# Performance work log

Hardware: AMD Instinct MI355X
Metric: run time of the kernel (lower is better)

The kernel has to match this reference:

```python
import jax, jax.numpy as jnp
import numpy as np

N, D, C, O = 65536, 256, 1024, 64

def setup_inputs() -> dict:
    key = jax.random.key(0)
    k1, k2, k3, k4 = jax.random.split(key, 4)
    x = jax.random.normal(k1, (N, D), dtype=jnp.float32)
    centers = jax.random.normal(k2, (C, D), dtype=jnp.float32)
    sigma = jnp.ones((C,), dtype=jnp.float32)
    # nn.Linear(C, O): weight [O, C], bias [O]
    bound = 1.0 / np.sqrt(C)
    W = jax.random.uniform(k3, (O, C), minval=-bound, maxval=bound, dtype=jnp.float32)
    b = jax.random.uniform(k4, (O,), minval=-bound, maxval=bound, dtype=jnp.float32)
    return {"x": x, "centers": centers, "sigma": sigma, "W": W, "b": b}

def reference(x, centers, sigma, W, b):
    # dist_sq[n,c] = ||x_n - c_c||^2, via GEMM identity (same math as sum((x-c)**2))
    x_sq = jnp.sum(x * x, axis=-1, keepdims=True)              # [N,1]
    c_sq = jnp.sum(centers * centers, axis=-1)                 # [C]
    cross = jnp.einsum('nd,cd->nc', x, centers)                # [N,C]
    dist_sq = x_sq - 2.0 * cross + c_sq[None, :]               # [N,C]
    rbf = jnp.exp(-dist_sq / (2.0 * sigma ** 2 + 1e-8))        # [N,C]
    out = jnp.einsum('nc,oc->no', rbf, W) + b                  # [N,O]
    return out
```

## Files before the change

kernel.cpp:

```cpp
#include <hip/hip_runtime.h>
#include <stdint.h>

#define NROWS 65536
#define DIM   256
#define NC    1024
#define NO    64

#define BN    128
#define WROWS 32
#define BC    64
#define NTILE (NC / BC)

using bf16x8 = __bf16 __attribute__((ext_vector_type(8)));
using f32x4  = float __attribute__((ext_vector_type(4)));
using u16x4  = unsigned short __attribute__((ext_vector_type(4)));
using u32x2  = unsigned int __attribute__((ext_vector_type(2)));

#define MFMA16(a, b, c) __builtin_amdgcn_mfma_f32_16x16x32_bf16((a), (b), (c), 0, 0, 0)

__device__ inline unsigned short bf16_bits(float f) {
    __bf16 h = (__bf16)f;
    return __builtin_bit_cast(unsigned short, h);
}


__global__ __launch_bounds__(256) void prep_cent(const float* __restrict__ cent,
                                                 const float* __restrict__ sigma,
                                                 unsigned short* __restrict__ cbf,
                                                 float* __restrict__ csq,
                                                 float* __restrict__ alpha) {
    const int wid = threadIdx.x >> 6, lane = threadIdx.x & 63;
    const int c = blockIdx.x * 4 + wid;
    float4 v = ((const float4*)cent)[(size_t)c * 64 + lane];
    u16x4 o;
    o[0] = bf16_bits(v.x); o[1] = bf16_bits(v.y);
    o[2] = bf16_bits(v.z); o[3] = bf16_bits(v.w);
    int byteoff = c * 512 + (((lane >> 1) * 16) ^ ((c & 7) << 4)) + (lane & 1) * 8;
    *(u16x4*)((char*)cbf + byteoff) = o;
    float ss = v.x * v.x + v.y * v.y + v.z * v.z + v.w * v.w;
    #pragma unroll
    for (int off = 32; off; off >>= 1) ss += __shfl_down(ss, off);
    if (lane == 0) {
        csq[c] = ss;
        float s = sigma[c];
        alpha[c] = 1.0f / (2.0f * s * s + 1e-8f);
    }
}

__global__ __launch_bounds__(256) void prep_w(const float* __restrict__ w,
                                              unsigned short* __restrict__ wbf) {
    const int o = blockIdx.x;
    float4 v = ((const float4*)w)[(size_t)o * 256 + threadIdx.x];
    u16x4 u;
    u[0] = bf16_bits(v.x); u[1] = bf16_bits(v.y);
    u[2] = bf16_bits(v.z); u[3] = bf16_bits(v.w);
    *(u16x4*)(wbf + (size_t)o * NC + threadIdx.x * 4) = u;
}

__global__ __launch_bounds__(256, 2) void rbf_main(
    const float* __restrict__ x,
    const __bf16* __restrict__ cbf, const float* __restrict__ csq,
    const float* __restrict__ alpha, const __bf16* __restrict__ wbf,
    const float* __restrict__ bias, float* __restrict__ out) {

    __shared__ __bf16 cent_lds[BC * DIM];
    __shared__ __bf16 rbf_lds[4][WROWS * BC];

    const int tid  = threadIdx.x;
    const int wid  = tid >> 6;
    const int lane = tid & 63;
    const int l15  = lane & 15;
    const int hi   = lane >> 4;

    const int rowbase = blockIdx.x * BN + wid * WROWS;

    bf16x8 xf[2][8];
    float xsqv[2];
    #pragma unroll
    for (int nf = 0; nf < 2; ++nf) {
        const float* xr = x + (size_t)(rowbase + nf * 16 + l15) * DIM;
        float ss = 0.f;
        #pragma unroll
        for (int ks = 0; ks < 8; ++ks) {
            float4 a = *(const float4*)(xr + ks * 32 + hi * 8);
            float4 b = *(const float4*)(xr + ks * 32 + hi * 8 + 4);
            bf16x8 f;
            f[0] = (__bf16)a.x; f[1] = (__bf16)a.y; f[2] = (__bf16)a.z; f[3] = (__bf16)a.w;
            f[4] = (__bf16)b.x; f[5] = (__bf16)b.y; f[6] = (__bf16)b.z; f[7] = (__bf16)b.w;
            xf[nf][ks] = f;
            ss += a.x * a.x + a.y * a.y + a.z * a.z + a.w * a.w;
            ss += b.x * b.x + b.y * b.y + b.z * b.z + b.w * b.w;
        }
        ss += __shfl_xor(ss, 16);
        ss += __shfl_xor(ss, 32);
        xsqv[nf] = ss;
    }

    float bo[4];
    #pragma unroll
    for (int of = 0; of < 4; ++of) bo[of] = bias[of * 16 + l15];

    f32x4 oacc[2][4];
    #pragma unroll
    for (int nf = 0; nf < 2; ++nf)
        #pragma unroll
        for (int of = 0; of < 4; ++of) {
            f32x4 z = {0.f, 0.f, 0.f, 0.f};
            oacc[nf][of] = z;
        }

    for (int t = 0; t < NTILE; ++t) {
        __syncthreads();
        {
            const __bf16* src = cbf + (size_t)t * BC * DIM;
            #pragma unroll
            for (int i = 0; i < 8; ++i) {
                const __bf16* g = src + (size_t)(i * 256 + tid) * 8;
                __bf16* l = (__bf16*)cent_lds + (i * 256 + (wid * 64)) * 8;
                __builtin_amdgcn_global_load_lds(
                    (const __attribute__((address_space(1))) uint32_t*)g,
                    (__attribute__((address_space(3))) uint32_t*)l, 16, 0, 0);
            }
        }
        asm volatile("s_waitcnt vmcnt(0)" ::: "memory");
        __syncthreads();

        f32x4 st[4][2];
        #pragma unroll
        for (int c4 = 0; c4 < 4; ++c4)
            #pragma unroll
            for (int nf = 0; nf < 2; ++nf) {
                f32x4 z = {0.f, 0.f, 0.f, 0.f};
                st[c4][nf] = z;
            }
        #pragma unroll
        for (int ks = 0; ks < 8; ++ks) {
            bf16x8 cf[4];
            #pragma unroll
            for (int c4 = 0; c4 < 4; ++c4) {
                const int crow = c4 * 16 + l15;
                const int byte = crow * 512 + ((ks * 64 + hi * 16) ^ ((crow & 7) << 4));
                cf[c4] = *(const bf16x8*)((const char*)cent_lds + byte);
            }
            #pragma unroll
            for (int c4 = 0; c4 < 4; ++c4)
                #pragma unroll
                for (int nf = 0; nf < 2; ++nf)
                    st[c4][nf] = MFMA16(cf[c4], xf[nf][ks], st[c4][nf]);
        }

        char* const rbase = (char*)&rbf_lds[wid][0];
        #pragma unroll
        for (int c4 = 0; c4 < 4; ++c4) {
            const int cl0 = c4 * 16 + hi * 4;
            const int cg  = t * BC + cl0;
            const f32x4 cs4 = *(const f32x4*)(csq + cg);
            const f32x4 al4 = *(const f32x4*)(alpha + cg);
            #pragma unroll
            for (int nf = 0; nf < 2; ++nf) {
                const f32x4 v = st[c4][nf];
                float p0 = __expf((2.0f * v[0] - xsqv[nf] - cs4[0]) * al4[0]);
                float p1 = __expf((2.0f * v[1] - xsqv[nf] - cs4[1]) * al4[1]);
                float p2 = __expf((2.0f * v[2] - xsqv[nf] - cs4[2]) * al4[2]);
                float p3 = __expf((2.0f * v[3] - xsqv[nf] - cs4[3]) * al4[3]);
                u32x2 wv;
                wv[0] = (unsigned)bf16_bits(p0) | ((unsigned)bf16_bits(p1) << 16);
                wv[1] = (unsigned)bf16_bits(p2) | ((unsigned)bf16_bits(p3) << 16);
                const int n = nf * 16 + l15;
                const int byte = (n * 128 + cl0 * 2) ^ ((n & 7) << 4);
                *(u32x2*)(rbase + byte) = wv;
            }
        }

        #pragma unroll
        for (int cs = 0; cs < 2; ++cs) {
            bf16x8 pa[2];
            #pragma unroll
            for (int nf = 0; nf < 2; ++nf) {
                const int n = nf * 16 + l15;
                const int byte = (n * 128 + cs * 64 + hi * 16) ^ ((n & 7) << 4);
                pa[nf] = *(const bf16x8*)((const char*)rbase + byte);
            }
            #pragma unroll
            for (int of = 0; of < 4; ++of) {
                const bf16x8 wb = *(const bf16x8*)(wbf + (size_t)(of * 16 + l15) * NC
                                                   + t * BC + cs * 32 + hi * 8);
                #pragma unroll
                for (int nf = 0; nf < 2; ++nf)
                    oacc[nf][of] = MFMA16(pa[nf], wb, oacc[nf][of]);
            }
        }
    }

    #pragma unroll
    for (int nf = 0; nf < 2; ++nf)
        #pragma unroll
        for (int of = 0; of < 4; ++of)
            #pragma unroll
            for (int r = 0; r < 4; ++r) {
                const int n = rowbase + nf * 16 + hi * 4 + r;
                out[(size_t)n * NO + of * 16 + l15] = oacc[nf][of][r] + bo[of];
            }
}

extern "C" void kernel_launch(void* const* d_in, const int* in_sizes, int n_in,
                              void* d_out, int out_size, void* d_ws, size_t ws_size,
                              hipStream_t stream) {
    const float* x     = (const float*)d_in[0];
    const float* cent  = (const float*)d_in[1];
    const float* sigma = (const float*)d_in[2];
    const float* W     = (const float*)d_in[3];
    const float* b     = (const float*)d_in[4];
    float* out = (float*)d_out;

    char* ws = (char*)d_ws;
    unsigned short* cbf  = (unsigned short*)(ws + 0);
    float*          csqp = (float*)(ws + 524288);
    float*          alp  = (float*)(ws + 528384);
    unsigned short* wbf  = (unsigned short*)(ws + 532480);

    prep_cent<<<NC / 4, 256, 0, stream>>>(cent, sigma, cbf, csqp, alp);
    prep_w<<<NO, 256, 0, stream>>>(W, wbf);
    rbf_main<<<NROWS / BN, 256, 0, stream>>>(
        x, (const __bf16*)cbf, csqp, alp, (const __bf16*)wbf, b, out);
}
```

Before: 162.5 us.

## Double-buffer center tiles, fold RBF scale constants, fuse prep kernels

```diff
diff --git a/kernel.cpp b/kernel.cpp
--- a/kernel.cpp
+++ b/kernel.cpp
@@ -23,47 +23,52 @@
     return __builtin_bit_cast(unsigned short, h);
 }
 
-
-__global__ __launch_bounds__(256) void prep_cent(const float* __restrict__ cent,
-                                                 const float* __restrict__ sigma,
-                                                 unsigned short* __restrict__ cbf,
-                                                 float* __restrict__ csq,
-                                                 float* __restrict__ alpha) {
-    const int wid = threadIdx.x >> 6, lane = threadIdx.x & 63;
-    const int c = blockIdx.x * 4 + wid;
-    float4 v = ((const float4*)cent)[(size_t)c * 64 + lane];
-    u16x4 o;
-    o[0] = bf16_bits(v.x); o[1] = bf16_bits(v.y);
-    o[2] = bf16_bits(v.z); o[3] = bf16_bits(v.w);
-    int byteoff = c * 512 + (((lane >> 1) * 16) ^ ((c & 7) << 4)) + (lane & 1) * 8;
-    *(u16x4*)((char*)cbf + byteoff) = o;
-    float ss = v.x * v.x + v.y * v.y + v.z * v.z + v.w * v.w;
-    #pragma unroll
-    for (int off = 32; off; off >>= 1) ss += __shfl_down(ss, off);
-    if (lane == 0) {
-        csq[c] = ss;
-        float s = sigma[c];
-        alpha[c] = 1.0f / (2.0f * s * s + 1e-8f);
+__global__ __launch_bounds__(256) void prep(const float* __restrict__ cent,
+                                            const float* __restrict__ sigma,
+                                            const float* __restrict__ w,
+                                            unsigned short* __restrict__ cbf,
+                                            float* __restrict__ a2,
+                                            float* __restrict__ aal,
+                                            float* __restrict__ acs,
+                                            unsigned short* __restrict__ wbf) {
+    const int bid = blockIdx.x;
+    if (bid < 256) {
+        const int wid = threadIdx.x >> 6, lane = threadIdx.x & 63;
+        const int c = bid * 4 + wid;
+        float4 v = ((const float4*)cent)[(size_t)c * 64 + lane];
+        u16x4 o;
+        o[0] = bf16_bits(v.x); o[1] = bf16_bits(v.y);
+        o[2] = bf16_bits(v.z); o[3] = bf16_bits(v.w);
+        const int t = c >> 6, crow = c & 63, kc = lane >> 1;
+        *(u16x4*)((char*)cbf + t * 32768 + (kc * 64 + crow) * 16 + (lane & 1) * 8) = o;
+        float ss = v.x * v.x + v.y * v.y + v.z * v.z + v.w * v.w;
+        #pragma unroll
+        for (int off = 32; off; off >>= 1) ss += __shfl_down(ss, off);
+        if (lane == 0) {
+            float s = sigma[c];
+            float al = 1.0f / (2.0f * s * s + 1e-8f);
+            a2[c] = 2.0f * al;
+            aal[c] = al;
+            acs[c] = al * ss;
+        }
+    } else {
+        const int o = bid - 256;
+        float4 v = ((const float4*)w)[(size_t)o * 256 + threadIdx.x];
+        u16x4 u;
+        u[0] = bf16_bits(v.x); u[1] = bf16_bits(v.y);
+        u[2] = bf16_bits(v.z); u[3] = bf16_bits(v.w);
+        *(u16x4*)(wbf + (size_t)o * NC + threadIdx.x * 4) = u;
     }
-}
-
-__global__ __launch_bounds__(256) void prep_w(const float* __restrict__ w,
-                                              unsigned short* __restrict__ wbf) {
-    const int o = blockIdx.x;
-    float4 v = ((const float4*)w)[(size_t)o * 256 + threadIdx.x];
-    u16x4 u;
-    u[0] = bf16_bits(v.x); u[1] = bf16_bits(v.y);
-    u[2] = bf16_bits(v.z); u[3] = bf16_bits(v.w);
-    *(u16x4*)(wbf + (size_t)o * NC + threadIdx.x * 4) = u;
 }
 
 __global__ __launch_bounds__(256, 2) void rbf_main(
     const float* __restrict__ x,
-    const __bf16* __restrict__ cbf, const float* __restrict__ csq,
-    const float* __restrict__ alpha, const __bf16* __restrict__ wbf,
+    const __bf16* __restrict__ cbf, const float* __restrict__ a2,
+    const float* __restrict__ aal, const float* __restrict__ acs,
+    const __bf16* __restrict__ wbf,
     const float* __restrict__ bias, float* __restrict__ out) {
 
-    __shared__ __bf16 cent_lds[BC * DIM];
+    __shared__ __bf16 cent_lds[2][BC * DIM];
     __shared__ __bf16 rbf_lds[4][WROWS * BC];
 
     const int tid  = threadIdx.x;
@@ -73,6 +78,19 @@
     const int hi   = lane >> 4;
 
     const int rowbase = blockIdx.x * BN + wid * WROWS;
+
+    auto stage = [&](int buf, int t) {
+        const char* src = (const char*)cbf + (size_t)t * 32768 + (size_t)(wid * 64 + lane) * 16;
+        char* dstb = (char*)&cent_lds[buf][0] + (wid * 64) * 16;
+        #pragma unroll
+        for (int i = 0; i < 8; ++i) {
+            __builtin_amdgcn_global_load_lds(
+                (const __attribute__((address_space(1))) uint32_t*)(src + i * 4096),
+                (__attribute__((address_space(3))) uint32_t*)(dstb + i * 4096), 16, 0, 0);
+        }
+    };
+
+    stage(0, 0);
 
     bf16x8 xf[2][8];
     float xsqv[2];
@@ -109,22 +127,15 @@
             oacc[nf][of] = z;
         }
 
+    asm volatile("s_waitcnt vmcnt(0)" ::: "memory");
+    __syncthreads();
+
+    int cur = 0;
+    #pragma unroll 1
     for (int t = 0; t < NTILE; ++t) {
-        __syncthreads();
-        {
-            const __bf16* src = cbf + (size_t)t * BC * DIM;
-            #pragma unroll
-            for (int i = 0; i < 8; ++i) {
-                const __bf16* g = src + (size_t)(i * 256 + tid) * 8;
-                __bf16* l = (__bf16*)cent_lds + (i * 256 + (wid * 64)) * 8;
-                __builtin_amdgcn_global_load_lds(
-                    (const __attribute__((address_space(1))) uint32_t*)g,
-                    (__attribute__((address_space(3))) uint32_t*)l, 16, 0, 0);
-            }
-        }
-        asm volatile("s_waitcnt vmcnt(0)" ::: "memory");
-        __syncthreads();
-
+        if (t + 1 < NTILE) stage(cur ^ 1, t + 1);
+
+        const char* cb = (const char*)&cent_lds[cur][0];
         f32x4 st[4][2];
         #pragma unroll
         for (int c4 = 0; c4 < 4; ++c4)
@@ -137,11 +148,8 @@
         for (int ks = 0; ks < 8; ++ks) {
             bf16x8 cf[4];
             #pragma unroll
-            for (int c4 = 0; c4 < 4; ++c4) {
-                const int crow = c4 * 16 + l15;
-                const int byte = crow * 512 + ((ks * 64 + hi * 16) ^ ((crow & 7) << 4));
-                cf[c4] = *(const bf16x8*)((const char*)cent_lds + byte);
-            }
+            for (int c4 = 0; c4 < 4; ++c4)
+                cf[c4] = *(const bf16x8*)(cb + ((ks * 4 + hi) * 64 + c4 * 16 + l15) * 16);
             #pragma unroll
             for (int c4 = 0; c4 < 4; ++c4)
                 #pragma unroll
@@ -152,22 +160,26 @@
         char* const rbase = (char*)&rbf_lds[wid][0];
         #pragma unroll
         for (int c4 = 0; c4 < 4; ++c4) {
-            const int cl0 = c4 * 16 + hi * 4;
-            const int cg  = t * BC + cl0;
-            const f32x4 cs4 = *(const f32x4*)(csq + cg);
-            const f32x4 al4 = *(const f32x4*)(alpha + cg);
+            const int cg = t * BC + c4 * 16 + hi * 4;
+            const f32x4 a24 = *(const f32x4*)(a2 + cg);
+            const f32x4 al4 = *(const f32x4*)(aal + cg);
+            const f32x4 ac4 = *(const f32x4*)(acs + cg);
             #pragma unroll
             for (int nf = 0; nf < 2; ++nf) {
                 const f32x4 v = st[c4][nf];
-                float p0 = __expf((2.0f * v[0] - xsqv[nf] - cs4[0]) * al4[0]);
-                float p1 = __expf((2.0f * v[1] - xsqv[nf] - cs4[1]) * al4[1]);
-                float p2 = __expf((2.0f * v[2] - xsqv[nf] - cs4[2]) * al4[2]);
-                float p3 = __expf((2.0f * v[3] - xsqv[nf] - cs4[3]) * al4[3]);
+                f32x4 t0;
+                t0[0] = -al4[0] * xsqv[nf] - ac4[0];
+                t0[1] = -al4[1] * xsqv[nf] - ac4[1];
+                t0[2] = -al4[2] * xsqv[nf] - ac4[2];
+                t0[3] = -al4[3] * xsqv[nf] - ac4[3];
+                float p0 = __expf(a24[0] * v[0] + t0[0]);
+                float p1 = __expf(a24[1] * v[1] + t0[1]);
+                float p2 = __expf(a24[2] * v[2] + t0[2]);
+                float p3 = __expf(a24[3] * v[3] + t0[3]);
                 u32x2 wv;
                 wv[0] = (unsigned)bf16_bits(p0) | ((unsigned)bf16_bits(p1) << 16);
                 wv[1] = (unsigned)bf16_bits(p2) | ((unsigned)bf16_bits(p3) << 16);
-                const int n = nf * 16 + l15;
-                const int byte = (n * 128 + cl0 * 2) ^ ((n & 7) << 4);
+                const int byte = ((c4 * 2 + (hi >> 1)) * 32 + nf * 16 + l15) * 16 + (hi & 1) * 8;
                 *(u32x2*)(rbase + byte) = wv;
             }
         }
@@ -176,11 +188,8 @@
         for (int cs = 0; cs < 2; ++cs) {
             bf16x8 pa[2];
             #pragma unroll
-            for (int nf = 0; nf < 2; ++nf) {
-                const int n = nf * 16 + l15;
-                const int byte = (n * 128 + cs * 64 + hi * 16) ^ ((n & 7) << 4);
-                pa[nf] = *(const bf16x8*)((const char*)rbase + byte);
-            }
+            for (int nf = 0; nf < 2; ++nf)
+                pa[nf] = *(const bf16x8*)(rbase + ((cs * 4 + hi) * 32 + nf * 16 + l15) * 16);
             #pragma unroll
             for (int of = 0; of < 4; ++of) {
                 const bf16x8 wb = *(const bf16x8*)(wbf + (size_t)(of * 16 + l15) * NC
@@ -190,6 +199,10 @@
                     oacc[nf][of] = MFMA16(pa[nf], wb, oacc[nf][of]);
             }
         }
+
+        asm volatile("s_waitcnt vmcnt(0)" ::: "memory");
+        __syncthreads();
+        cur ^= 1;
     }
 
     #pragma unroll
@@ -215,12 +228,12 @@
 
     char* ws = (char*)d_ws;
     unsigned short* cbf  = (unsigned short*)(ws + 0);
-    float*          csqp = (float*)(ws + 524288);
-    float*          alp  = (float*)(ws + 528384);
-    unsigned short* wbf  = (unsigned short*)(ws + 532480);
-
-    prep_cent<<<NC / 4, 256, 0, stream>>>(cent, sigma, cbf, csqp, alp);
-    prep_w<<<NO, 256, 0, stream>>>(W, wbf);
+    float*          a2p  = (float*)(ws + 524288);
+    float*          aalp = (float*)(ws + 528384);
+    float*          acsp = (float*)(ws + 532480);
+    unsigned short* wbf  = (unsigned short*)(ws + 536576);
+
+    prep<<<320, 256, 0, stream>>>(cent, sigma, W, cbf, a2p, aalp, acsp, wbf);
     rbf_main<<<NROWS / BN, 256, 0, stream>>>(
-        x, (const __bf16*)cbf, csqp, alp, (const __bf16*)wbf, b, out);
-}
+        x, (const __bf16*)cbf, a2p, aalp, acsp, (const __bf16*)wbf, b, out);
+}
```

New measurement: 177.5 us. 9.2% more time.
